# Kernel optimization log

Measured on AMD Instinct MI355X. Metric: run time of the kernel, lower is better.

## Reference

```python
import jax, jax.numpy as jnp
import numpy as np

RES = (20, 20)
SIGMA = 0.1


def setup_inputs() -> dict:
    key = jax.random.key(0)
    # [batch, num_dims, max_points, 2] birth/death coords in [0,1)
    pd = jax.random.uniform(key, (32, 3, 2048, 2), dtype=jnp.float32)
    return {"persistence_diagrams": pd}


def reference(persistence_diagrams) -> jnp.ndarray:
    # births/deaths: [B, D, P]
    births = persistence_diagrams[..., 0]
    deaths = persistence_diagrams[..., 1]
    pers = deaths - births  # persistence; also the default weight function
    # Original loop skips all-zero rows and points with persistence <= 0.
    # An all-zero row has persistence == 0, so (pers > 0) subsumes both checks.
    eff_w = jnp.where(pers > 0, pers, 0.0)  # [B, D, P]

    x_range = jnp.linspace(0.0, 1.0, RES[0], dtype=jnp.float32)
    y_range = jnp.linspace(0.0, 1.0, RES[1], dtype=jnp.float32)
    xx, yy = jnp.meshgrid(x_range, y_range, indexing="ij")  # [Rx, Ry]

    # Splat each point's Gaussian centered at (birth, persistence) onto the grid.
    # d2: [B, D, P, Rx, Ry]
    d2 = (xx - births[..., None, None]) ** 2 + (yy - pers[..., None, None]) ** 2
    gauss = jnp.exp(-d2 / (2.0 * SIGMA ** 2))
    # Weighted sum over points -> [B, D, Rx, Ry]
    image = jnp.einsum("bdpxy,bdp->bdxy", gauss, eff_w)
    return image
```

## Files before the change

kernel.cpp:

```cpp
#include <hip/hip_runtime.h>


#define RX 20
#define RY 20
#define SPLIT 8
#define CHUNK 256
#define PST 260

__global__ __launch_bounds__(256) void pimg_kernel(const float2* __restrict__ pd,
                                                   float* __restrict__ out,
                                                   int n_bd) {
    __shared__ __attribute__((aligned(16))) float s_gxT[RX * PST];
    __shared__ __attribute__((aligned(16))) float s_gyT[RY * PST];
    __shared__ int s_wave_cnt[4];
    __shared__ float s_red[100 * 5];

    const int tid   = threadIdx.x;
    const int bd    = blockIdx.x / SPLIT;
    const int chunk = blockIdx.x % SPLIT;
    const int pbase = bd * 2048 + chunk * CHUNK;

    float2 p2  = pd[pbase + tid];
    float birth = p2.x;
    float pers  = p2.y - p2.x;
    bool active = pers > 0.0f;

    unsigned long long mask = __ballot(active);
    int lane = tid & 63;
    int wid  = tid >> 6;
    int rank = __popcll(mask & ((1ull << lane) - 1ull));
    if (lane == 0) s_wave_cnt[wid] = __popcll(mask);
    __syncthreads();

    int offset = 0;
    #pragma unroll
    for (int w = 0; w < 4; ++w)
        if (w < wid) offset += s_wave_cnt[w];
    int total = s_wave_cnt[0] + s_wave_cnt[1] + s_wave_cnt[2] + s_wave_cnt[3];
    int tp = (total + 3) & ~3;

    if (active) {
        int slot = offset + rank;
        #pragma unroll
        for (int i = 0; i < RX; ++i) {
            float xi = i * (1.0f / 19.0f);
            float dx = xi - birth;
            float dy = xi - pers;
            s_gxT[i * PST + slot] = pers * __expf(-50.0f * dx * dx);
            s_gyT[i * PST + slot] =        __expf(-50.0f * dy * dy);
        }
    }
    if (tid >= total && tid < tp) {
        #pragma unroll
        for (int i = 0; i < RX; ++i) {
            s_gxT[i * PST + tid] = 0.0f;
            s_gyT[i * PST + tid] = 0.0f;
        }
    }
    __syncthreads();

    const int half = tid >> 7;
    const int t100 = tid & 127;
    float a00 = 0.0f, a01 = 0.0f, a10 = 0.0f, a11 = 0.0f;
    int ig = 0, jg = 0;
    if (t100 < 100) {
        ig = t100 / 10;
        jg = t100 % 10;
        int s_mid = (tp >> 1) & ~3;
        int s0 = half ? s_mid : 0;
        int s1 = half ? tp    : s_mid;
        const float* gxa = &s_gxT[ ig       * PST];
        const float* gxb = &s_gxT[(ig + 10) * PST];
        const float* gya = &s_gyT[ jg       * PST];
        const float* gyb = &s_gyT[(jg + 10) * PST];
        for (int s = s0; s < s1; s += 4) {
            float4 xa = *(const float4*)(gxa + s);
            float4 xb = *(const float4*)(gxb + s);
            float4 ya = *(const float4*)(gya + s);
            float4 yb = *(const float4*)(gyb + s);
            a00 = fmaf(xa.x, ya.x, a00); a00 = fmaf(xa.y, ya.y, a00);
            a00 = fmaf(xa.z, ya.z, a00); a00 = fmaf(xa.w, ya.w, a00);
            a01 = fmaf(xa.x, yb.x, a01); a01 = fmaf(xa.y, yb.y, a01);
            a01 = fmaf(xa.z, yb.z, a01); a01 = fmaf(xa.w, yb.w, a01);
            a10 = fmaf(xb.x, ya.x, a10); a10 = fmaf(xb.y, ya.y, a10);
            a10 = fmaf(xb.z, ya.z, a10); a10 = fmaf(xb.w, ya.w, a10);
            a11 = fmaf(xb.x, yb.x, a11); a11 = fmaf(xb.y, yb.y, a11);
            a11 = fmaf(xb.z, yb.z, a11); a11 = fmaf(xb.w, yb.w, a11);
        }
    }
    if (half == 1 && t100 < 100) {
        s_red[t100 * 5 + 0] = a00;
        s_red[t100 * 5 + 1] = a01;
        s_red[t100 * 5 + 2] = a10;
        s_red[t100 * 5 + 3] = a11;
    }
    __syncthreads();
    if (half == 0 && t100 < 100) {
        a00 += s_red[t100 * 5 + 0];
        a01 += s_red[t100 * 5 + 1];
        a10 += s_red[t100 * 5 + 2];
        a11 += s_red[t100 * 5 + 3];
        float* o = out + bd * (RX * RY);
        atomicAdd(o +  ig       * RY + jg,      a00);
        atomicAdd(o +  ig       * RY + jg + 10, a01);
        atomicAdd(o + (ig + 10) * RY + jg,      a10);
        atomicAdd(o + (ig + 10) * RY + jg + 10, a11);
    }
}

extern "C" void kernel_launch(void* const* d_in, const int* in_sizes, int n_in,
                              void* d_out, int out_size, void* d_ws, size_t ws_size,
                              hipStream_t stream) {
    const float2* pd = (const float2*)d_in[0];
    float* out = (float*)d_out;
    int n_bd = in_sizes[0] / (2048 * 2);
    hipMemsetAsync(d_out, 0, (size_t)out_size * sizeof(float), stream);
    pimg_kernel<<<dim3(n_bd * SPLIT), dim3(256), 0, stream>>>(pd, out, n_bd);
}
```

Before: 59.00 us.

## Restructure blocks to own half-images, loop over chunks, drop atomics and memset

```diff
diff --git a/kernel.cpp b/kernel.cpp
--- a/kernel.cpp
+++ b/kernel.cpp
@@ -3,108 +3,119 @@
 
 #define RX 20
 #define RY 20
-#define SPLIT 8
-#define CHUNK 256
-#define PST 260
+#define NPTS 2048
+#define THREADS 512
+#define CHUNK 512
+#define NCHUNK (NPTS / CHUNK)
+#define PST 516
 
-__global__ __launch_bounds__(256) void pimg_kernel(const float2* __restrict__ pd,
-                                                   float* __restrict__ out,
-                                                   int n_bd) {
+__global__ __launch_bounds__(THREADS) void pimg_kernel(const float2* __restrict__ pd,
+                                                       float* __restrict__ out) {
     __shared__ __attribute__((aligned(16))) float s_gxT[RX * PST];
     __shared__ __attribute__((aligned(16))) float s_gyT[RY * PST];
-    __shared__ int s_wave_cnt[4];
-    __shared__ float s_red[100 * 5];
+    __shared__ float2 s_pts[CHUNK];
+    __shared__ float  s_red[7 * 250];
+    __shared__ int    s_wave_cnt[8];
 
-    const int tid   = threadIdx.x;
-    const int bd    = blockIdx.x / SPLIT;
-    const int chunk = blockIdx.x % SPLIT;
-    const int pbase = bd * 2048 + chunk * CHUNK;
+    const int tid  = threadIdx.x;
+    const int bd   = blockIdx.x >> 1;
+    const int ih   = blockIdx.x & 1;
+    const int lane = tid & 63;
+    const int wid  = tid >> 6;
 
-    float2 p2  = pd[pbase + tid];
-    float birth = p2.x;
-    float pers  = p2.y - p2.x;
-    bool active = pers > 0.0f;
+    const float2* base = pd + bd * NPTS;
+    float2 p[NCHUNK];
+    #pragma unroll
+    for (int k = 0; k < NCHUNK; ++k) p[k] = base[k * CHUNK + tid];
 
-    unsigned long long mask = __ballot(active);
-    int lane = tid & 63;
-    int wid  = tid >> 6;
-    int rank = __popcll(mask & ((1ull << lane) - 1ull));
-    if (lane == 0) s_wave_cnt[wid] = __popcll(mask);
-    __syncthreads();
+    const int i0 = ih * 10 + (lane / 10);
+    const int j0 = lane % 10;
+    float a00 = 0.0f, a01 = 0.0f, a10 = 0.0f, a11 = 0.0f;
 
-    int offset = 0;
-    #pragma unroll
-    for (int w = 0; w < 4; ++w)
-        if (w < wid) offset += s_wave_cnt[w];
-    int total = s_wave_cnt[0] + s_wave_cnt[1] + s_wave_cnt[2] + s_wave_cnt[3];
-    int tp = (total + 3) & ~3;
+    for (int c = 0; c < NCHUNK; ++c) {
+        float birth = p[c].x;
+        float pers  = p[c].y - p[c].x;
+        bool active = pers > 0.0f;
+        unsigned long long mask = __ballot(active);
+        if (lane == 0) s_wave_cnt[wid] = __popcll(mask);
+        __syncthreads();
 
-    if (active) {
-        int slot = offset + rank;
+        int offset = 0, total = 0;
         #pragma unroll
-        for (int i = 0; i < RX; ++i) {
-            float xi = i * (1.0f / 19.0f);
-            float dx = xi - birth;
-            float dy = xi - pers;
-            s_gxT[i * PST + slot] = pers * __expf(-50.0f * dx * dx);
-            s_gyT[i * PST + slot] =        __expf(-50.0f * dy * dy);
+        for (int w = 0; w < 8; ++w) {
+            int cnt = s_wave_cnt[w];
+            if (w < wid) offset += cnt;
+            total += cnt;
         }
+        int tp = (total + 3) & ~3;
+        if (active) {
+            int rank = __popcll(mask & ((1ull << lane) - 1ull));
+            s_pts[offset + rank] = make_float2(birth, pers);
+        }
+        if (tid >= total && tid < tp)
+            s_pts[tid] = make_float2(0.0f, 0.0f);
+        __syncthreads();
+
+        {
+            const int ibase = (tid & 1) * 10;
+            for (int s = tid >> 1; s < tp; s += THREADS / 2) {
+                float2 bp = s_pts[s];
+                float b = bp.x, q = bp.y;
+                #pragma unroll
+                for (int ii = 0; ii < 10; ++ii) {
+                    int i = ibase + ii;
+                    float xi = i * (1.0f / 19.0f);
+                    float dx = xi - b;
+                    float dy = xi - q;
+                    s_gxT[i * PST + s] = q * __expf(-50.0f * dx * dx);
+                    s_gyT[i * PST + s] =     __expf(-50.0f * dy * dy);
+                }
+            }
+        }
+        __syncthreads();
+
+        if (lane < 50) {
+            int qs = (((tp + 7) >> 3) + 3) & ~3;
+            int s0 = wid * qs; if (s0 > tp) s0 = tp;
+            int s1 = s0 + qs;  if (s1 > tp) s1 = tp;
+            const float* gxa = &s_gxT[ i0       * PST];
+            const float* gxb = &s_gxT[(i0 + 5)  * PST];
+            const float* gya = &s_gyT[ j0       * PST];
+            const float* gyb = &s_gyT[(j0 + 10) * PST];
+            for (int s = s0; s < s1; s += 4) {
+                float4 xa = *(const float4*)(gxa + s);
+                float4 xb = *(const float4*)(gxb + s);
+                float4 ya = *(const float4*)(gya + s);
+                float4 yb = *(const float4*)(gyb + s);
+                a00 = fmaf(xa.x, ya.x, a00); a00 = fmaf(xa.y, ya.y, a00);
+                a00 = fmaf(xa.z, ya.z, a00); a00 = fmaf(xa.w, ya.w, a00);
+                a01 = fmaf(xa.x, yb.x, a01); a01 = fmaf(xa.y, yb.y, a01);
+                a01 = fmaf(xa.z, yb.z, a01); a01 = fmaf(xa.w, yb.w, a01);
+                a10 = fmaf(xb.x, ya.x, a10); a10 = fmaf(xb.y, ya.y, a10);
+                a10 = fmaf(xb.z, ya.z, a10); a10 = fmaf(xb.w, ya.w, a10);
+                a11 = fmaf(xb.x, yb.x, a11); a11 = fmaf(xb.y, yb.y, a11);
+                a11 = fmaf(xb.z, yb.z, a11); a11 = fmaf(xb.w, yb.w, a11);
+            }
+        }
+        __syncthreads();
     }
-    if (tid >= total && tid < tp) {
-        #pragma unroll
-        for (int i = 0; i < RX; ++i) {
-            s_gxT[i * PST + tid] = 0.0f;
-            s_gyT[i * PST + tid] = 0.0f;
-        }
+
+    if (wid > 0 && lane < 50) {
+        float* r = &s_red[(wid - 1) * 250 + lane * 5];
+        r[0] = a00; r[1] = a01; r[2] = a10; r[3] = a11;
     }
     __syncthreads();
-
-    const int half = tid >> 7;
-    const int t100 = tid & 127;
-    float a00 = 0.0f, a01 = 0.0f, a10 = 0.0f, a11 = 0.0f;
-    int ig = 0, jg = 0;
-    if (t100 < 100) {
-        ig = t100 / 10;
-        jg = t100 % 10;
-        int s_mid = (tp >> 1) & ~3;
-        int s0 = half ? s_mid : 0;
-        int s1 = half ? tp    : s_mid;
-        const float* gxa = &s_gxT[ ig       * PST];
-        const float* gxb = &s_gxT[(ig + 10) * PST];
-        const float* gya = &s_gyT[ jg       * PST];
-        const float* gyb = &s_gyT[(jg + 10) * PST];
-        for (int s = s0; s < s1; s += 4) {
-            float4 xa = *(const float4*)(gxa + s);
-            float4 xb = *(const float4*)(gxb + s);
-            float4 ya = *(const float4*)(gya + s);
-            float4 yb = *(const float4*)(gyb + s);
-            a00 = fmaf(xa.x, ya.x, a00); a00 = fmaf(xa.y, ya.y, a00);
-            a00 = fmaf(xa.z, ya.z, a00); a00 = fmaf(xa.w, ya.w, a00);
-            a01 = fmaf(xa.x, yb.x, a01); a01 = fmaf(xa.y, yb.y, a01);
-            a01 = fmaf(xa.z, yb.z, a01); a01 = fmaf(xa.w, yb.w, a01);
-            a10 = fmaf(xb.x, ya.x, a10); a10 = fmaf(xb.y, ya.y, a10);
-            a10 = fmaf(xb.z, ya.z, a10); a10 = fmaf(xb.w, ya.w, a10);
-            a11 = fmaf(xb.x, yb.x, a11); a11 = fmaf(xb.y, yb.y, a11);
-            a11 = fmaf(xb.z, yb.z, a11); a11 = fmaf(xb.w, yb.w, a11);
+    if (wid == 0 && lane < 50) {
+        #pragma unroll
+        for (int w = 0; w < 7; ++w) {
+            const float* r = &s_red[w * 250 + lane * 5];
+            a00 += r[0]; a01 += r[1]; a10 += r[2]; a11 += r[3];
         }
-    }
-    if (half == 1 && t100 < 100) {
-        s_red[t100 * 5 + 0] = a00;
-        s_red[t100 * 5 + 1] = a01;
-        s_red[t100 * 5 + 2] = a10;
-        s_red[t100 * 5 + 3] = a11;
-    }
-    __syncthreads();
-    if (half == 0 && t100 < 100) {
-        a00 += s_red[t100 * 5 + 0];
-        a01 += s_red[t100 * 5 + 1];
-        a10 += s_red[t100 * 5 + 2];
-        a11 += s_red[t100 * 5 + 3];
         float* o = out + bd * (RX * RY);
-        atomicAdd(o +  ig       * RY + jg,      a00);
-        atomicAdd(o +  ig       * RY + jg + 10, a01);
-        atomicAdd(o + (ig + 10) * RY + jg,      a10);
-        atomicAdd(o + (ig + 10) * RY + jg + 10, a11);
+        o[ i0       * RY + j0]      = a00;
+        o[ i0       * RY + j0 + 10] = a01;
+        o[(i0 + 5)  * RY + j0]      = a10;
+        o[(i0 + 5)  * RY + j0 + 10] = a11;
     }
 }
 
@@ -114,6 +125,5 @@
     const float2* pd = (const float2*)d_in[0];
     float* out = (float*)d_out;
     int n_bd = in_sizes[0] / (2048 * 2);
-    hipMemsetAsync(d_out, 0, (size_t)out_size * sizeof(float), stream);
-    pimg_kernel<<<dim3(n_bd * SPLIT), dim3(256), 0, stream>>>(pd, out, n_bd);
+    pimg_kernel<<<dim3(n_bd * 2), dim3(THREADS), 0, stream>>>(pd, out);
 }
```

Result: slower. 61.80 us (+4.7%).
